# Performance work log

Measured on AMD Instinct MI355X. Metric: run time of the kernel, lower is better.

The kernel has to match this reference:

```python
import jax, jax.numpy as jnp
import numpy as np

NFILT = 40          # mel filters
NBINS = 257         # nfft//2 + 1
HID = 64            # myconfig.LSTM_HIDDEN_SIZE
NLAYERS = 3         # myconfig.LSTM_NUM_LAYERS
B, T = 64, 2000


def setup_inputs() -> dict:
    key = jax.random.key(0)
    ks = jax.random.split(key, 16)
    x = jax.random.uniform(ks[0], (B, T, NBINS), jnp.float32)  # nonneg spectrogram-like
    # torch init: sorted randint(1, 257, (nfilt+2,)); sample w/o replacement -> distinct integer edges
    binpoints = jnp.sort(jax.random.permutation(ks[1], jnp.arange(1, 257))[:NFILT + 2]).astype(jnp.float32)
    s = 1.0 / np.sqrt(HID)
    def u(k, shape):
        return jax.random.uniform(k, shape, jnp.float32, -s, s)
    inp = {"x": x, "binpoints": binpoints}
    in_sizes = [NFILT, 2 * HID, 2 * HID]
    for l in range(NLAYERS):
        inp[f"w_ih_{l}"] = u(ks[2 + 4 * l], (2, 4 * HID, in_sizes[l]))
        inp[f"w_hh_{l}"] = u(ks[3 + 4 * l], (2, 4 * HID, HID))
        inp[f"b_ih_{l}"] = u(ks[4 + 4 * l], (2, 4 * HID))
        inp[f"b_hh_{l}"] = u(ks[5 + 4 * l], (2, 4 * HID))
    return inp


def make_fbank(binpoints):
    """Vectorized version of the torch double loop (one pass of broadcasted comparisons)."""
    b = jnp.sort(binpoints)                       # (42,)
    bj, bj1, bj2 = b[:NFILT], b[1:NFILT + 1], b[2:NFILT + 2]
    fb = jnp.floor(b)                             # int() truncation in torch loop bounds
    i = jnp.arange(NBINS, dtype=b.dtype)[None, :]  # (1, 257)
    rise_m = (i >= fb[:NFILT, None]) & (i < fb[1:NFILT + 1, None])
    fall_m = (i >= fb[1:NFILT + 1, None]) & (i < fb[2:NFILT + 2, None])
    d1 = bj1 - bj
    d2 = bj2 - bj1
    rise_v = (i - bj[:, None]) / jnp.where(d1 > 0, d1, 1.0)[:, None] ** 2
    fall_v = (bj2[:, None] - i) / jnp.where(d2 > 0, d2, 1.0)[:, None] ** 2
    fbank = jnp.where(fall_m, fall_v, jnp.where(rise_m, rise_v, 0.0))
    # torch loop runs j in range(nfilt-1): last filter row never written
    fbank = fbank * (jnp.arange(NFILT) < NFILT - 1)[:, None]
    return fbank


def lstm_dir(x, w_ih, w_hh, b_ih, b_hh, reverse):
    xs = jnp.flip(x, 1) if reverse else x
    pre = jnp.einsum('btd,gd->btg', xs, w_ih) + b_ih + b_hh  # (B, T, 4H)
    h0 = jnp.zeros((x.shape[0], HID), x.dtype)

    def step(carry, p):
        h, c = carry
        g = p + h @ w_hh.T
        ig, fg, gg, og = jnp.split(g, 4, axis=-1)  # torch gate order i,f,g,o
        c = jax.nn.sigmoid(fg) * c + jax.nn.sigmoid(ig) * jnp.tanh(gg)
        h = jax.nn.sigmoid(og) * jnp.tanh(c)
        return (h, c), h

    _, ys = jax.lax.scan(step, (h0, h0), jnp.swapaxes(pre, 0, 1))
    ys = jnp.swapaxes(ys, 0, 1)  # (B, T, H)
    return jnp.flip(ys, 1) if reverse else ys


def reference(x, binpoints, w_ih_0, w_hh_0, b_ih_0, b_hh_0,
              w_ih_1, w_hh_1, b_ih_1, b_hh_1,
              w_ih_2, w_hh_2, b_ih_2, b_hh_2):
    fbank = make_fbank(binpoints)                       # (40, 257)
    filt = jnp.einsum('btn,fn->btf', x, fbank)          # x @ fbank.T
    filt = filt.at[:, :, 0].set(x[:, :, 0])             # keep first column
    # remove_zero_rows is an identity here: no frame has an all-zero feature sum
    h = jnp.log(filt + 1e-10)
    params = [(w_ih_0, w_hh_0, b_ih_0, b_hh_0),
              (w_ih_1, w_hh_1, b_ih_1, b_hh_1),
              (w_ih_2, w_hh_2, b_ih_2, b_hh_2)]
    for (wi, wh, bi, bh) in params:  # bidirectional, 3 layers
        fwd = lstm_dir(h, wi[0], wh[0], bi[0], bh[0], False)
        bwd = lstm_dir(h, wi[1], wh[1], bi[1], bh[1], True)
        h = jnp.concatenate([fwd, bwd], axis=-1)        # (B, T, 2H)
    return jnp.mean(h, axis=1)                          # FRAME_AGGREGATION_MEAN
```

## Files before the change

kernel.cpp:

```cpp
#include <hip/hip_runtime.h>
#include <cstdint>
#include <cstddef>

#define NFILT 40
#define NBINS 257
#define HID   64
#define BB    64
#define TT    2000
#define GATES 256
#define MTOT  (BB*TT)

__device__ __forceinline__ float sigm(float x) {
  return 1.0f / (1.0f + __expf(-x));
}

__device__ __forceinline__ float bfly1(float x) {
  int i = __builtin_amdgcn_mov_dpp(__float_as_int(x), 0xB1, 0xF, 0xF, true);
  return x + __int_as_float(i);
}
__device__ __forceinline__ float bfly2(float x) {
  int i = __builtin_amdgcn_mov_dpp(__float_as_int(x), 0x4E, 0xF, 0xF, true);
  return x + __int_as_float(i);
}
#define QB(x, ctrl) __int_as_float(__builtin_amdgcn_mov_dpp(__float_as_int(x), (ctrl), 0xF, 0xF, true))

__device__ __forceinline__ float dot16(const float4* w, float4 a, float4 b,
                                       float4 c2, float4 d2, float acc) {
  acc = fmaf(a.x, w[0].x, acc);  acc = fmaf(a.y, w[0].y, acc);
  acc = fmaf(a.z, w[0].z, acc);  acc = fmaf(a.w, w[0].w, acc);
  acc = fmaf(b.x, w[1].x, acc);  acc = fmaf(b.y, w[1].y, acc);
  acc = fmaf(b.z, w[1].z, acc);  acc = fmaf(b.w, w[1].w, acc);
  acc = fmaf(c2.x, w[2].x, acc); acc = fmaf(c2.y, w[2].y, acc);
  acc = fmaf(c2.z, w[2].z, acc); acc = fmaf(c2.w, w[2].w, acc);
  acc = fmaf(d2.x, w[3].x, acc); acc = fmaf(d2.y, w[3].y, acc);
  acc = fmaf(d2.z, w[3].z, acc); acc = fmaf(d2.w, w[3].w, acc);
  return acc;
}

__global__ void k_fbank(const float* __restrict__ binpoints,
                        float* __restrict__ fbank,
                        int* __restrict__ lohi ) {
  __shared__ float b[NFILT + 2];
  int tid = threadIdx.x;
  if (tid < NFILT + 2) b[tid] = binpoints[tid];
  __syncthreads();
  if (tid < NFILT) {
    if (tid == NFILT - 1) { lohi[tid] = 0; lohi[NFILT + tid] = 0; }
    else {
      int lo = (int)floorf(b[tid]);
      int hi = (int)floorf(b[tid + 2]);
      if (lo < 0) lo = 0;
      if (hi > NBINS) hi = NBINS;
      lohi[tid] = lo; lohi[NFILT + tid] = hi;
    }
  }
  for (int idx = tid; idx < NFILT * NBINS; idx += blockDim.x) {
    int f = idx / NBINS, i = idx - f * NBINS;
    float bj = b[f], bj1 = b[f + 1], bj2 = b[f + 2];
    float fb0 = floorf(bj), fb1 = floorf(bj1), fb2 = floorf(bj2);
    float fi = (float)i;
    bool rise = (fi >= fb0) && (fi < fb1);
    bool fall = (fi >= fb1) && (fi < fb2);
    float d1 = bj1 - bj;  d1 = (d1 > 0.f) ? d1 : 1.f;
    float d2 = bj2 - bj1; d2 = (d2 > 0.f) ? d2 : 1.f;
    float rv = (fi - bj)  / (d1 * d1);
    float fv = (bj2 - fi) / (d2 * d2);
    float v = fall ? fv : (rise ? rv : 0.f);
    if (f == NFILT - 1) v = 0.f;
    fbank[idx] = v;
  }
}

__global__ __launch_bounds__(64) void k_feat(const float* __restrict__ x,
                                             const float* __restrict__ fbank,
                                             const int* __restrict__ lohi,
                                             float* __restrict__ h0) {
  int bt = blockIdx.x;
  __shared__ float xs[NBINS];
  const float* xr = x + (size_t)bt * NBINS;
  for (int i = threadIdx.x; i < NBINS; i += 64) xs[i] = xr[i];
  __syncthreads();
  int f = threadIdx.x;
  if (f < NFILT) {
    float acc = 0.f;
    int lo = lohi[f], hi = lohi[NFILT + f];
    for (int i = lo; i < hi; ++i) acc = fmaf(xs[i], fbank[f * NBINS + i], acc);
    float val = (f == 0) ? xs[0] : acc;
    h0[(size_t)bt * NFILT + f] = logf(val + 1e-10f);
  }
}

template <int K, int BK>
__global__ __launch_bounds__(256) void k_gemm(const float* __restrict__ Hm,
                                              const float* __restrict__ W,
                                              const float* __restrict__ bih,
                                              const float* __restrict__ bhh,
                                              float* __restrict__ pre) {
  constexpr int BM = 128, BN = 128;
  __shared__ float Hs[BK][BM + 4];
  __shared__ float Ws[BK][BN + 4];
  const int d  = blockIdx.z;
  const int m0 = blockIdx.x * BM;
  const int g0 = blockIdx.y * BN;
  const int tid = threadIdx.x;
  const int tx = tid & 15, ty = tid >> 4;

  float acc[8][8];
#pragma unroll
  for (int r = 0; r < 8; ++r)
#pragma unroll
    for (int j = 0; j < 8; ++j) acc[r][j] = 0.f;

  for (int k0 = 0; k0 < K; k0 += BK) {
    constexpr int HL = BM * BK / 256;
#pragma unroll
    for (int i = 0; i < HL; ++i) {
      int flat = tid + i * 256;
      int r = flat / BK, kk = flat - r * BK;
      Hs[kk][r] = Hm[(size_t)(m0 + r) * K + k0 + kk];
    }
    constexpr int WL = BN * BK / 256;
#pragma unroll
    for (int i = 0; i < WL; ++i) {
      int flat = tid + i * 256;
      int r = flat / BK, kk = flat - r * BK;
      Ws[kk][r] = W[((size_t)d * GATES + g0 + r) * K + k0 + kk];
    }
    __syncthreads();
#pragma unroll
    for (int kk = 0; kk < BK; ++kk) {
      const float4 wv0 = *(const float4*)&Ws[kk][tx * 8];
      const float4 wv1 = *(const float4*)&Ws[kk][tx * 8 + 4];
      const float4 hv0 = *(const float4*)&Hs[kk][ty * 8];
      const float4 hv1 = *(const float4*)&Hs[kk][ty * 8 + 4];
      const float hr[8] = {hv0.x, hv0.y, hv0.z, hv0.w, hv1.x, hv1.y, hv1.z, hv1.w};
      const float wc[8] = {wv0.x, wv0.y, wv0.z, wv0.w, wv1.x, wv1.y, wv1.z, wv1.w};
#pragma unroll
      for (int r = 0; r < 8; ++r)
#pragma unroll
        for (int j = 0; j < 8; ++j)
          acc[r][j] = fmaf(hr[r], wc[j], acc[r][j]);
    }
    __syncthreads();
  }

  const int gcol = g0 + tx * 8;
  float bsum[8];
#pragma unroll
  for (int i = 0; i < 8; ++i)
    bsum[i] = bih[d * GATES + gcol + i] + bhh[d * GATES + gcol + i];
#pragma unroll
  for (int r = 0; r < 8; ++r) {
    size_t m = (size_t)(m0 + ty * 8 + r);
    float4 o0 = {acc[r][0] + bsum[0], acc[r][1] + bsum[1], acc[r][2] + bsum[2], acc[r][3] + bsum[3]};
    float4 o1 = {acc[r][4] + bsum[4], acc[r][5] + bsum[5], acc[r][6] + bsum[6], acc[r][7] + bsum[7]};
    *(float4*)&pre[((size_t)d * MTOT + m) * GATES + gcol] = o0;
    *(float4*)&pre[((size_t)d * MTOT + m) * GATES + gcol + 4] = o1;
  }
}

__global__ __attribute__((amdgpu_waves_per_eu(1, 1)))
__launch_bounds__(256) void k_lstmq(const float* __restrict__ pre,
                                    const float* __restrict__ whh,
                                    float* __restrict__ hout,
                                    float* __restrict__ out,
                                    int final_layer) {
  const int b   = blockIdx.x;
  const int d   = blockIdx.y;
  const int tid = threadIdx.x;
  const int wl  = tid >> 6;
  const int l   = tid & 63;
  const int uu  = wl * 16 + (l >> 2);
  const int p   = l & 3;
  const int p16 = p * 16;

  __shared__ __align__(16) float hs[2][HID];

  float4 wq[4][4];
#pragma unroll
  for (int q = 0; q < 4; ++q) {
    const float4* wr = (const float4*)(whh + ((size_t)d * GATES + q * HID + uu) * HID + p16);
#pragma unroll
    for (int c2 = 0; c2 < 4; ++c2) wq[q][c2] = wr[c2];
  }
  {
    float* wf = (float*)&wq[0][0];
#pragma unroll
    for (int i = 0; i < 64; ++i) asm volatile("" : "+v"(wf[i]));
  }
  const float sA = (p == 2) ? 2.f : 1.f;
  const float aA = (p == 2) ? 2.f : 1.f;
  const float aB = (p == 2) ? -1.f : 0.f;
  const bool  p1 = (p & 1) != 0;
  const bool  p2 = (p & 2) != 0;

  if (tid < HID) { hs[0][tid] = 0.f; hs[1][tid] = 0.f; }
  float c = 0.f, sum = 0.f;
  __syncthreads();

  const int t0 = d ? (TT - 1) : 0;
  const int dt = d ? -1 : 1;
  const float* pp = pre + ((size_t)d * MTOT + (size_t)b * TT + t0) * GATES + (p * HID + uu);
  const ptrdiff_t pstr = (ptrdiff_t)dt * GATES;

  float pf0 = pp[0], pf1 = pp[pstr], pf2 = pp[pstr * 2], pf3 = pp[pstr * 3];

#define LSTM_STEP(TK, PAR, PF)                                                  \
  do {                                                                          \
    const float4* h4 = (const float4*)&hs[PAR][p16];                            \
    const float4 hA = h4[0], hB = h4[1], hC = h4[2], hD = h4[3];                \
    float a0 = dot16(wq[0], hA, hB, hC, hD, 0.f);                               \
    float a1 = dot16(wq[1], hA, hB, hC, hD, 0.f);                               \
    float a2 = dot16(wq[2], hA, hB, hC, hD, 0.f);                               \
    float a3 = dot16(wq[3], hA, hB, hC, hD, 0.f);                               \
    a0 = bfly2(bfly1(a0)); a1 = bfly2(bfly1(a1));                               \
    a2 = bfly2(bfly1(a2)); a3 = bfly2(bfly1(a3));                               \
    const float t02 = p2 ? a2 : a0;                                             \
    const float t13 = p2 ? a3 : a1;                                             \
    const float zsel = (p1 ? t13 : t02) + (PF);                                 \
    const float act = fmaf(sigm(zsel * sA), aA, aB);                            \
    const float ig = QB(act, 0x00), fg = QB(act, 0x55);                         \
    const float gg = QB(act, 0xAA), og = QB(act, 0xFF);                         \
    c = fmaf(fg, c, ig * gg);                                                   \
    const float tc = fmaf(sigm(2.f * c), 2.f, -1.f);                            \
    const float hvv = og * tc;                                                  \
    if (p == 0) hs[(PAR) ^ 1][uu] = hvv;                                        \
    asm volatile("s_waitcnt lgkmcnt(0)\n\ts_barrier" ::: "memory");             \
    if (final_layer) sum += hvv;                                                \
    else if (p == 0)                                                            \
      hout[((size_t)b * TT + (size_t)(t0 + dt * (TK))) * (2 * HID) + d * HID + uu] = hvv; \
  } while (0)

  for (int t = 0; t < TT; t += 4) {
    LSTM_STEP(t + 0, 0, pf0);
    { int ip = t + 4; if (ip >= TT) ip = 0; pf0 = pp[pstr * (ptrdiff_t)ip]; }
    LSTM_STEP(t + 1, 1, pf1);
    { int ip = t + 5; if (ip >= TT) ip = 0; pf1 = pp[pstr * (ptrdiff_t)ip]; }
    LSTM_STEP(t + 2, 0, pf2);
    { int ip = t + 6; if (ip >= TT) ip = 0; pf2 = pp[pstr * (ptrdiff_t)ip]; }
    LSTM_STEP(t + 3, 1, pf3);
    { int ip = t + 7; if (ip >= TT) ip = 0; pf3 = pp[pstr * (ptrdiff_t)ip]; }
  }
#undef LSTM_STEP

  if (final_layer && p == 0) out[b * (2 * HID) + d * HID + uu] = sum * (1.0f / (float)TT);
}

extern "C" void kernel_launch(void* const* d_in, const int* in_sizes, int n_in,
                              void* d_out, int out_size, void* d_ws, size_t ws_size,
                              hipStream_t stream) {
  const float* x         = (const float*)d_in[0];
  const float* binpoints = (const float*)d_in[1];
  const float* w_ih[3] = {(const float*)d_in[2], (const float*)d_in[6],  (const float*)d_in[10]};
  const float* w_hh[3] = {(const float*)d_in[3], (const float*)d_in[7],  (const float*)d_in[11]};
  const float* b_ih[3] = {(const float*)d_in[4], (const float*)d_in[8],  (const float*)d_in[12]};
  const float* b_hh[3] = {(const float*)d_in[5], (const float*)d_in[9],  (const float*)d_in[13]};
  float* out = (float*)d_out;

  float* pre   = (float*)d_ws;
  float* Hbuf  = pre  + (size_t)2 * MTOT * GATES;
  float* h0    = Hbuf + (size_t)MTOT * 128;
  float* fbank = h0   + (size_t)MTOT * NFILT;
  int*   lohi  = (int*)(fbank + NFILT * NBINS);

  k_fbank<<<1, 256, 0, stream>>>(binpoints, fbank, lohi);
  k_feat<<<MTOT, 64, 0, stream>>>(x, fbank, lohi, h0);

  k_gemm<40, 40><<<dim3(MTOT / 128, GATES / 128, 2), 256, 0, stream>>>(h0, w_ih[0], b_ih[0], b_hh[0], pre);
  k_lstmq<<<dim3(BB, 2), 256, 0, stream>>>(pre, w_hh[0], Hbuf, out, 0);

  k_gemm<128, 32><<<dim3(MTOT / 128, GATES / 128, 2), 256, 0, stream>>>(Hbuf, w_ih[1], b_ih[1], b_hh[1], pre);
  k_lstmq<<<dim3(BB, 2), 256, 0, stream>>>(pre, w_hh[1], Hbuf, out, 0);

  k_gemm<128, 32><<<dim3(MTOT / 128, GATES / 128, 2), 256, 0, stream>>>(Hbuf, w_ih[2], b_ih[2], b_hh[2], pre);
  k_lstmq<<<dim3(BB, 2), 256, 0, stream>>>(pre, w_hh[2], Hbuf, out, 1);
}
```

Before: 3.140 ms.

## Merge LSTM directions into one 512-thread block and shrink GEMM N-tile

The recurrent kernel now runs both directions of a sequence in one 512-thread block. Each half uses its own shared h buffer, and the grid drops from 128 blocks to 64. Separately, the input-projection GEMM tile shrinks from 128x128 to 128x64, which halves each thread's accumulators and doubles the number of blocks, aiming at higher occupancy. The shared barrier now couples the two directions, so each direction waits for the other every step. Packing two directions per CU also changes the wave-per-EU budget from 1 to 2, which may pressure registers holding the 64 weight values.

```diff
diff --git a/kernel.cpp b/kernel.cpp
--- a/kernel.cpp
+++ b/kernel.cpp
@@ -96,7 +96,7 @@
                                               const float* __restrict__ bih,
                                               const float* __restrict__ bhh,
                                               float* __restrict__ pre) {
-  constexpr int BM = 128, BN = 128;
+  constexpr int BM = 128, BN = 64;
   __shared__ float Hs[BK][BM + 4];
   __shared__ float Ws[BK][BN + 4];
   const int d  = blockIdx.z;
@@ -105,11 +105,11 @@
   const int tid = threadIdx.x;
   const int tx = tid & 15, ty = tid >> 4;
 
-  float acc[8][8];
+  float acc[8][4];
 #pragma unroll
   for (int r = 0; r < 8; ++r)
 #pragma unroll
-    for (int j = 0; j < 8; ++j) acc[r][j] = 0.f;
+    for (int j = 0; j < 4; ++j) acc[r][j] = 0.f;
 
   for (int k0 = 0; k0 < K; k0 += BK) {
     constexpr int HL = BM * BK / 256;
@@ -129,52 +129,49 @@
     __syncthreads();
 #pragma unroll
     for (int kk = 0; kk < BK; ++kk) {
-      const float4 wv0 = *(const float4*)&Ws[kk][tx * 8];
-      const float4 wv1 = *(const float4*)&Ws[kk][tx * 8 + 4];
+      const float4 wv  = *(const float4*)&Ws[kk][tx * 4];
       const float4 hv0 = *(const float4*)&Hs[kk][ty * 8];
       const float4 hv1 = *(const float4*)&Hs[kk][ty * 8 + 4];
       const float hr[8] = {hv0.x, hv0.y, hv0.z, hv0.w, hv1.x, hv1.y, hv1.z, hv1.w};
-      const float wc[8] = {wv0.x, wv0.y, wv0.z, wv0.w, wv1.x, wv1.y, wv1.z, wv1.w};
-#pragma unroll
-      for (int r = 0; r < 8; ++r)
-#pragma unroll
-        for (int j = 0; j < 8; ++j)
-          acc[r][j] = fmaf(hr[r], wc[j], acc[r][j]);
+#pragma unroll
+      for (int r = 0; r < 8; ++r) {
+        acc[r][0] = fmaf(hr[r], wv.x, acc[r][0]);
+        acc[r][1] = fmaf(hr[r], wv.y, acc[r][1]);
+        acc[r][2] = fmaf(hr[r], wv.z, acc[r][2]);
+        acc[r][3] = fmaf(hr[r], wv.w, acc[r][3]);
+      }
     }
     __syncthreads();
   }
 
-  const int gcol = g0 + tx * 8;
-  float bsum[8];
-#pragma unroll
-  for (int i = 0; i < 8; ++i)
-    bsum[i] = bih[d * GATES + gcol + i] + bhh[d * GATES + gcol + i];
+  const int gcol = g0 + tx * 4;
+  const float4 bi = *(const float4*)&bih[d * GATES + gcol];
+  const float4 bh = *(const float4*)&bhh[d * GATES + gcol];
+  const float bx = bi.x + bh.x, by = bi.y + bh.y, bz = bi.z + bh.z, bw = bi.w + bh.w;
 #pragma unroll
   for (int r = 0; r < 8; ++r) {
     size_t m = (size_t)(m0 + ty * 8 + r);
-    float4 o0 = {acc[r][0] + bsum[0], acc[r][1] + bsum[1], acc[r][2] + bsum[2], acc[r][3] + bsum[3]};
-    float4 o1 = {acc[r][4] + bsum[4], acc[r][5] + bsum[5], acc[r][6] + bsum[6], acc[r][7] + bsum[7]};
-    *(float4*)&pre[((size_t)d * MTOT + m) * GATES + gcol] = o0;
-    *(float4*)&pre[((size_t)d * MTOT + m) * GATES + gcol + 4] = o1;
-  }
-}
-
-__global__ __attribute__((amdgpu_waves_per_eu(1, 1)))
-__launch_bounds__(256) void k_lstmq(const float* __restrict__ pre,
+    float4 o = {acc[r][0] + bx, acc[r][1] + by, acc[r][2] + bz, acc[r][3] + bw};
+    *(float4*)&pre[((size_t)d * MTOT + m) * GATES + gcol] = o;
+  }
+}
+
+__global__ __attribute__((amdgpu_waves_per_eu(2, 2)))
+__launch_bounds__(512) void k_lstmq(const float* __restrict__ pre,
                                     const float* __restrict__ whh,
                                     float* __restrict__ hout,
                                     float* __restrict__ out,
                                     int final_layer) {
   const int b   = blockIdx.x;
-  const int d   = blockIdx.y;
   const int tid = threadIdx.x;
-  const int wl  = tid >> 6;
+  const int d   = tid >> 8;
+  const int wl  = (tid >> 6) & 3;
   const int l   = tid & 63;
   const int uu  = wl * 16 + (l >> 2);
   const int p   = l & 3;
   const int p16 = p * 16;
 
-  __shared__ __align__(16) float hs[2][HID];
+  __shared__ __align__(16) float hs[2][2][HID];
 
   float4 wq[4][4];
 #pragma unroll
@@ -194,7 +191,7 @@
   const bool  p1 = (p & 1) != 0;
   const bool  p2 = (p & 2) != 0;
 
-  if (tid < HID) { hs[0][tid] = 0.f; hs[1][tid] = 0.f; }
+  if ((tid & 255) < HID) { hs[d][0][tid & 63] = 0.f; hs[d][1][tid & 63] = 0.f; }
   float c = 0.f, sum = 0.f;
   __syncthreads();
 
@@ -207,7 +204,7 @@
 
 #define LSTM_STEP(TK, PAR, PF)                                                  \
   do {                                                                          \
-    const float4* h4 = (const float4*)&hs[PAR][p16];                            \
+    const float4* h4 = (const float4*)&hs[d][PAR][p16];                         \
     const float4 hA = h4[0], hB = h4[1], hC = h4[2], hD = h4[3];                \
     float a0 = dot16(wq[0], hA, hB, hC, hD, 0.f);                               \
     float a1 = dot16(wq[1], hA, hB, hC, hD, 0.f);                               \
@@ -224,7 +221,7 @@
     c = fmaf(fg, c, ig * gg);                                                   \
     const float tc = fmaf(sigm(2.f * c), 2.f, -1.f);                            \
     const float hvv = og * tc;                                                  \
-    if (p == 0) hs[(PAR) ^ 1][uu] = hvv;                                        \
+    if (p == 0) hs[d][(PAR) ^ 1][uu] = hvv;                                     \
     asm volatile("s_waitcnt lgkmcnt(0)\n\ts_barrier" ::: "memory");             \
     if (final_layer) sum += hvv;                                                \
     else if (p == 0)                                                            \
@@ -266,12 +263,12 @@
   k_fbank<<<1, 256, 0, stream>>>(binpoints, fbank, lohi);
   k_feat<<<MTOT, 64, 0, stream>>>(x, fbank, lohi, h0);
 
-  k_gemm<40, 40><<<dim3(MTOT / 128, GATES / 128, 2), 256, 0, stream>>>(h0, w_ih[0], b_ih[0], b_hh[0], pre);
-  k_lstmq<<<dim3(BB, 2), 256, 0, stream>>>(pre, w_hh[0], Hbuf, out, 0);
-
-  k_gemm<128, 32><<<dim3(MTOT / 128, GATES / 128, 2), 256, 0, stream>>>(Hbuf, w_ih[1], b_ih[1], b_hh[1], pre);
-  k_lstmq<<<dim3(BB, 2), 256, 0, stream>>>(pre, w_hh[1], Hbuf, out, 0);
-
-  k_gemm<128, 32><<<dim3(MTOT / 128, GATES / 128, 2), 256, 0, stream>>>(Hbuf, w_ih[2], b_ih[2], b_hh[2], pre);
-  k_lstmq<<<dim3(BB, 2), 256, 0, stream>>>(pre, w_hh[2], Hbuf, out, 1);
-}
+  k_gemm<40, 40><<<dim3(MTOT / 128, GATES / 64, 2), 256, 0, stream>>>(h0, w_ih[0], b_ih[0], b_hh[0], pre);
+  k_lstmq<<<BB, 512, 0, stream>>>(pre, w_hh[0], Hbuf, out, 0);
+
+  k_gemm<128, 32><<<dim3(MTOT / 128, GATES / 64, 2), 256, 0, stream>>>(Hbuf, w_ih[1], b_ih[1], b_hh[1], pre);
+  k_lstmq<<<BB, 512, 0, stream>>>(pre, w_hh[1], Hbuf, out, 0);
+
+  k_gemm<128, 32><<<dim3(MTOT / 128, GATES / 64, 2), 256, 0, stream>>>(Hbuf, w_ih[2], b_ih[2], b_hh[2], pre);
+  k_lstmq<<<BB, 512, 0, stream>>>(pre, w_hh[2], Hbuf, out, 1);
+}
```

Result: slower. 3.695 ms (+17.7%).
